# Kernel optimization log

Hardware: AMD Instinct MI355X
Metric: run time of the kernel (lower is better)

Reference implementation:

```python
import jax, jax.numpy as jnp
import numpy as np

K = 4096       # in_features (reduction dim)
N = 11008      # out_features
GROUP = 128    # scale group size along K
PACK = 8       # int4 values per int32


def dequantize_int4(packed, scales):
    """packed: [K//8, N] int32 (8 int4 nibbles per word along K),
    scales: [K//GROUP, N] fp16. Returns fp16 weight [K, N] with
    w = (nibble - 8) * scale (symmetric zero-point-8 scheme)."""
    shifts = (jnp.arange(PACK, dtype=jnp.int32) * 4)
    # [K//8, 8, N] -> [K, N]
    nibbles = (packed[:, None, :] >> shifts[None, :, None]) & 0xF
    q = nibbles.reshape(K, N)
    s = jnp.repeat(scales, GROUP, axis=0)  # [K, N]
    return (q.astype(jnp.float16) - jnp.float16(8.0)) * s


def setup_inputs() -> dict:
    key = jax.random.key(0)
    k1, k2, k3, k4 = jax.random.split(key, 4)
    x = jax.random.normal(k1, (4, 1024, K), dtype=jnp.float16)
    packed = jax.random.randint(k2, (K // PACK, N), 0, 2147483647, dtype=jnp.int32)
    scales = (jax.random.uniform(k3, (K // GROUP, N), dtype=jnp.float32) * 0.02 + 0.001).astype(jnp.float16)
    bias = jax.random.normal(k4, (N,), dtype=jnp.float16)
    return {"x": x, "packed": packed, "scales": scales, "bias": bias}


def reference(x, packed, scales, bias):
    in_shape = x.shape
    x2 = x.reshape(-1, in_shape[-1]).astype(jnp.float16)  # [M, K]
    w = dequantize_int4(packed, scales)                    # [K, N]
    out = jnp.matmul(x2, w)                                # [M, N] fp16
    out = out.reshape(*in_shape[:-1], -1)
    return out + bias
```

## Files before the change

kernel.cpp:

```cpp
#include <hip/hip_runtime.h>
#include <hip/hip_bf16.h>
#include <stdint.h>

#define K_DIM 4096
#define N_DIM 11008
#define BM 128
#define BN 256
#define NT (K_DIM / 64)

typedef _Float16 half8 __attribute__((ext_vector_type(8)));
typedef _Float16 half2v __attribute__((ext_vector_type(2)));
typedef float floatx4 __attribute__((ext_vector_type(4)));

typedef const uint32_t __attribute__((address_space(1)))* gas_u32p;
typedef uint32_t __attribute__((address_space(3)))* las_u32p;

__device__ __forceinline__ void glds16(const void* g, void* l) {
    __builtin_amdgcn_global_load_lds((gas_u32p)g, (las_u32p)l, 16, 0, 0);
}

__device__ __forceinline__ half8 dequant_word_pk(uint32_t w, half2v s2) {
    const uint32_t M = 0x000F000Fu;
    const uint32_t B = 0x64006400u;
    union { uint32_t u; half2v h; } t0, t1, t2, t3;
    t0.u = (w & M) | B;
    t1.u = ((w >> 4) & M) | B;
    t2.u = ((w >> 8) & M) | B;
    t3.u = ((w >> 12) & M) | B;
    const half2v off = {(_Float16)1032.0f, (_Float16)1032.0f};
    union { half8 h8; half2v h2[4]; } o;
    o.h2[0] = (t0.h - off) * s2;
    o.h2[1] = (t1.h - off) * s2;
    o.h2[2] = (t2.h - off) * s2;
    o.h2[3] = (t3.h - off) * s2;
    return o.h8;
}

__device__ __forceinline__ half8 dequant_word_f16(uint32_t w, float s) {
    half8 r;
    #pragma unroll
    for (int j = 0; j < 8; ++j) {
        int q = (int)((w >> (4 * j)) & 0xFu);
        r[j] = (_Float16)((float)(q - 8) * s);
    }
    return r;
}

__global__ __launch_bounds__(256)
void cvt_kernel(const float* __restrict__ X, _Float16* __restrict__ Xh) {
    size_t idx = (size_t)blockIdx.x * 256 + threadIdx.x;
    size_t base = idx * 8;
    floatx4 a = __builtin_nontemporal_load((const floatx4*)(X + base));
    floatx4 b = __builtin_nontemporal_load((const floatx4*)(X + base + 4));
    half8 h;
    h[0] = (_Float16)a[0]; h[1] = (_Float16)b[0];
    h[2] = (_Float16)a[1]; h[3] = (_Float16)b[1];
    h[4] = (_Float16)a[2]; h[5] = (_Float16)b[2];
    h[6] = (_Float16)a[3]; h[7] = (_Float16)b[3];
    *(half8*)(Xh + base) = h;
}

__global__ __launch_bounds__(256, 2)
void qgemm_lds(const _Float16* __restrict__ Xh,
               const int* __restrict__ Wp,
               const float* __restrict__ Sc,
               const float* __restrict__ Bias,
               float* __restrict__ Out)
{
    __shared__ half8 As[3][BM * 8];

    const int tid = threadIdx.x;

    const int bid = blockIdx.y * gridDim.x + blockIdx.x;
    const int xcd = bid & 7;
    const int k_r = bid >> 3;
    const int m0 = (xcd * 4 + (k_r & 3)) * BM;
    const int n0 = (k_r >> 2) * BN;

    const int lane = tid & 63;
    const int wid  = tid >> 6;
    const int wn   = wid;
    const int q    = lane >> 4;
    const int tt   = lane & 15;

    const int arow = tid >> 3;
    const int ac   = (tid & 7) ^ (arow & 7);
    const _Float16* aSrc = Xh + (size_t)(m0 + arow) * K_DIM + ac * 8;

    const int ncol = n0 + wn * 64 + tt;
    const int* bPtr = Wp + (size_t)q * N_DIM + ncol;
    const float* scPtr = Sc + ncol;

    floatx4 acc[8][4];
    #pragma unroll
    for (int i = 0; i < 8; ++i)
        #pragma unroll
        for (int j = 0; j < 4; ++j)
            acc[i][j] = floatx4{0.f, 0.f, 0.f, 0.f};

    const int x7  = tt & 7;
    const int rb0 = tt * 128 + ((0 * 4 + q) ^ x7) * 16;
    const int rb1 = tt * 128 + ((1 * 4 + q) ^ x7) * 16;

    char* pr = (char*)As[0];
    char* pm = (char*)As[1];
    char* pw = (char*)As[2];

    #pragma unroll
    for (int i = 0; i < 4; ++i)
        glds16(aSrc + (size_t)i * 32 * K_DIM,
               pr + (size_t)(i * 256 + tid) * 16);
    __builtin_amdgcn_sched_barrier(0);

    half2v s2[4], sn2[4];
    #pragma unroll
    for (int j = 0; j < 4; ++j) {
        _Float16 sh = (_Float16)scPtr[j * 16];
        s2[j] = (half2v){sh, sh};
    }
    uint32_t wv[8];
    #pragma unroll
    for (int ks = 0; ks < 2; ++ks)
        #pragma unroll
        for (int j = 0; j < 4; ++j)
            wv[ks * 4 + j] = (uint32_t)bPtr[(size_t)(ks * 4) * N_DIM + j * 16];
    __builtin_amdgcn_sched_barrier(0);

    #pragma unroll
    for (int i = 0; i < 4; ++i)
        glds16(aSrc + (size_t)i * 32 * K_DIM + 64,
               pm + (size_t)(i * 256 + tid) * 16);
    __builtin_amdgcn_sched_barrier(0);

    asm volatile("s_waitcnt vmcnt(16)" ::: "memory");
    __builtin_amdgcn_s_barrier();
    __builtin_amdgcn_sched_barrier(0);

    for (int kt = 0; kt < NT; ++kt) {
        if (kt > 0 && (kt & 1) == 0) {
            #pragma unroll
            for (int j = 0; j < 4; ++j) s2[j] = sn2[j];
        }

        half8 bf[8];
        #pragma unroll
        for (int ks = 0; ks < 2; ++ks)
            #pragma unroll
            for (int j = 0; j < 4; ++j)
                bf[ks * 4 + j] = dequant_word_pk(wv[ks * 4 + j], s2[j]);

        if (kt + 1 < NT) {
            const int* bp = bPtr + (size_t)(kt + 1) * 8 * N_DIM;
            #pragma unroll
            for (int ks = 0; ks < 2; ++ks)
                #pragma unroll
                for (int j = 0; j < 4; ++j)
                    wv[ks * 4 + j] = (uint32_t)bp[(size_t)(ks * 4) * N_DIM + j * 16];
            if (kt & 1) {
                const float* sp = scPtr + (size_t)((kt + 1) >> 1) * N_DIM;
                #pragma unroll
                for (int j = 0; j < 4; ++j) {
                    _Float16 sh = (_Float16)sp[j * 16];
                    sn2[j] = (half2v){sh, sh};
                }
            }
        }
        __builtin_amdgcn_sched_barrier(0);

        if (kt + 2 < NT) {
            #pragma unroll
            for (int i = 0; i < 4; ++i)
                glds16(aSrc + (size_t)i * 32 * K_DIM + (kt + 2) * 64,
                       pw + (size_t)(i * 256 + tid) * 16);
        }
        __builtin_amdgcn_sched_barrier(0);

        #pragma unroll
        for (int ks = 0; ks < 2; ++ks) {
            const int rb = ks ? rb1 : rb0;
            #pragma unroll
            for (int i = 0; i < 8; ++i) {
                half8 af = *(const half8*)(pr + rb + i * 2048);
                #pragma unroll
                for (int j = 0; j < 4; ++j)
                    acc[i][j] = __builtin_amdgcn_mfma_f32_16x16x32_f16(
                        af, bf[ks * 4 + j], acc[i][j], 0, 0, 0);
            }
        }

        if (kt + 1 < NT) {
            if (kt + 2 < NT) {
                if (kt & 1) { asm volatile("s_waitcnt vmcnt(16)" ::: "memory"); }
                else        { asm volatile("s_waitcnt vmcnt(12)" ::: "memory"); }
            } else {
                asm volatile("s_waitcnt vmcnt(8)" ::: "memory");
            }
            __builtin_amdgcn_s_barrier();
            __builtin_amdgcn_sched_barrier(0);
        }

        char* t = pr; pr = pm; pm = pw; pw = t;
    }

    #pragma unroll
    for (int j = 0; j < 4; ++j) {
        const int n = ncol + j * 16;
        const float bv = Bias[n];
        #pragma unroll
        for (int i = 0; i < 8; ++i) {
            const int mrow = m0 + i * 16 + q * 4;
            #pragma unroll
            for (int r = 0; r < 4; ++r)
                Out[(size_t)(mrow + r) * N_DIM + n] = acc[i][j][r] + bv;
        }
    }
}

__global__ __launch_bounds__(256, 2)
void qgemm_direct(const float* __restrict__ X,
                  const int* __restrict__ Wp,
                  const float* __restrict__ Sc,
                  const float* __restrict__ Bias,
                  float* __restrict__ Out)
{
    const int tid = threadIdx.x;
    const int m0 = blockIdx.x * 256;
    const int n0 = blockIdx.y * 128;
    const int lane = tid & 63;
    const int wid  = tid >> 6;
    const int wm   = wid >> 1;
    const int wn   = wid & 1;
    const int q    = lane >> 4;
    const int tt   = lane & 15;

    const int ncol = n0 + wn * 64 + tt;
    const int* bPtr = Wp + (size_t)q * N_DIM + ncol;
    const float* scPtr = Sc + ncol;
    const float* aBase = X + (size_t)(m0 + wm * 128 + tt) * K_DIM + q * 8;

    floatx4 acc[8][4];
    #pragma unroll
    for (int i = 0; i < 8; ++i)
        #pragma unroll
        for (int j = 0; j < 4; ++j)
            acc[i][j] = floatx4{0.f, 0.f, 0.f, 0.f};

    float s[4];
    for (int kt = 0; kt < NT; ++kt) {
        if ((kt & 1) == 0) {
            const float* sp = scPtr + (size_t)(kt >> 1) * N_DIM;
            #pragma unroll
            for (int j = 0; j < 4; ++j) s[j] = sp[j * 16];
        }
        const int* bp = bPtr + (size_t)kt * 8 * N_DIM;
        uint32_t wv[8];
        #pragma unroll
        for (int ks = 0; ks < 2; ++ks)
            #pragma unroll
            for (int j = 0; j < 4; ++j)
                wv[ks * 4 + j] = (uint32_t)bp[(size_t)(ks * 4) * N_DIM + j * 16];
        half8 bf[8];
        #pragma unroll
        for (int ks = 0; ks < 2; ++ks)
            #pragma unroll
            for (int j = 0; j < 4; ++j)
                bf[ks * 4 + j] = dequant_word_f16(wv[ks * 4 + j], s[j]);
        #pragma unroll
        for (int ks = 0; ks < 2; ++ks) {
            const size_t ko = (size_t)(kt * 64 + ks * 32);
            #pragma unroll
            for (int i = 0; i < 8; ++i) {
                const float* ap = aBase + (size_t)i * 16 * K_DIM + ko;
                floatx4 lo = *(const floatx4*)ap;
                floatx4 hi = *(const floatx4*)(ap + 4);
                half8 af;
                af[0] = (_Float16)lo[0]; af[1] = (_Float16)lo[1];
                af[2] = (_Float16)lo[2]; af[3] = (_Float16)lo[3];
                af[4] = (_Float16)hi[0]; af[5] = (_Float16)hi[1];
                af[6] = (_Float16)hi[2]; af[7] = (_Float16)hi[3];
                #pragma unroll
                for (int j = 0; j < 4; ++j)
                    acc[i][j] = __builtin_amdgcn_mfma_f32_16x16x32_f16(
                        af, bf[ks * 4 + j], acc[i][j], 0, 0, 0);
            }
        }
    }
    #pragma unroll
    for (int j = 0; j < 4; ++j) {
        const int n = ncol + j * 16;
        const float bv = Bias[n];
        #pragma unroll
        for (int i = 0; i < 8; ++i) {
            const int mrow = m0 + wm * 128 + i * 16 + q * 4;
            #pragma unroll
            for (int r = 0; r < 4; ++r)
                Out[(size_t)(mrow + r) * N_DIM + n] = acc[i][j][r] + bv;
        }
    }
}

extern "C" void kernel_launch(void* const* d_in, const int* in_sizes, int n_in,
                              void* d_out, int out_size, void* d_ws, size_t ws_size,
                              hipStream_t stream) {
    (void)in_sizes; (void)n_in; (void)out_size;
    const float* X    = (const float*)d_in[0];
    const int*   Wp   = (const int*)d_in[1];
    const float* Sc   = (const float*)d_in[2];
    const float* Bias = (const float*)d_in[3];
    float*       Out  = (float*)d_out;

    const size_t needed = (size_t)4096 * K_DIM * sizeof(_Float16);

    if (ws_size >= needed) {
        _Float16* Xh = (_Float16*)d_ws;
        cvt_kernel<<<(4096 * K_DIM) / (256 * 8), 256, 0, stream>>>(X, Xh);
        dim3 grid(4096 / BM, N_DIM / BN);
        qgemm_lds<<<grid, 256, 0, stream>>>(Xh, Wp, Sc, Bias, Out);
    } else {
        dim3 gridf(4096 / 256, N_DIM / 128);
        qgemm_direct<<<gridf, 256, 0, stream>>>(X, Wp, Sc, Bias, Out);
    }
}
```

Before: 604.6 us.

## Split K-tile into four interleaved phases with barriers and MFMA priority

Restructures the main K loop of the LDS GEMM into four sub-phases per tile. Each phase interleaves A-fragment LDS reads, next-tile weight loads, one global-to-LDS copy and dequantization with a 4x4 MFMA block. Phases are separated by workgroup barriers and raise wave priority around the MFMAs, in a ping-pong style meant to overlap memory and compute across the two waves per SIMD. Weight registers are double-buffered by unrolling the loop by two. The extra barriers add synchronization overhead and may stall if the waves do not interleave well.

```diff
diff --git a/kernel.cpp b/kernel.cpp
--- a/kernel.cpp
+++ b/kernel.cpp
@@ -60,6 +60,143 @@
     *(half8*)(Xh + base) = h;
 }
 
+__device__ __forceinline__ void tile_body(
+    int kt, uint32_t (&wvC)[8], uint32_t (&wvN)[8],
+    half2v (&s2)[4], half2v (&sn2)[4],
+    floatx4 (&acc)[8][4],
+    char*& pr, char*& pm, char*& pw,
+    const _Float16* aSrc, const int* bPtr, const float* scPtr,
+    int rb0, int rb1, int tid)
+{
+    if (kt > 0 && (kt & 1) == 0) {
+        #pragma unroll
+        for (int j = 0; j < 4; ++j) s2[j] = sn2[j];
+    }
+
+    const int* bp = bPtr + (size_t)(kt + 1) * 8 * N_DIM;
+    half8 bf[4];
+    half8 af[4];
+
+    #pragma unroll
+    for (int i = 0; i < 4; ++i)
+        af[i] = *(const half8*)(pr + rb0 + i * 2048);
+    if (kt + 1 < NT) {
+        #pragma unroll
+        for (int j = 0; j < 4; ++j)
+            wvN[j] = (uint32_t)bp[j * 16];
+    }
+    if (kt + 2 < NT)
+        glds16(aSrc + (size_t)(kt + 2) * 64,
+               pw + (size_t)tid * 16);
+    #pragma unroll
+    for (int j = 0; j < 4; ++j)
+        bf[j] = dequant_word_pk(wvC[j], s2[j]);
+    __builtin_amdgcn_sched_barrier(0);
+    __builtin_amdgcn_s_barrier();
+    asm volatile("s_waitcnt lgkmcnt(0)" ::: "memory");
+    __builtin_amdgcn_sched_barrier(0);
+    __builtin_amdgcn_s_setprio(1);
+    #pragma unroll
+    for (int i = 0; i < 4; ++i)
+        #pragma unroll
+        for (int j = 0; j < 4; ++j)
+            acc[i][j] = __builtin_amdgcn_mfma_f32_16x16x32_f16(
+                af[i], bf[j], acc[i][j], 0, 0, 0);
+    __builtin_amdgcn_s_setprio(0);
+    __builtin_amdgcn_sched_barrier(0);
+    __builtin_amdgcn_s_barrier();
+
+    #pragma unroll
+    for (int i = 0; i < 4; ++i)
+        af[i] = *(const half8*)(pr + rb0 + (4 + i) * 2048);
+    if (kt + 1 < NT) {
+        #pragma unroll
+        for (int j = 0; j < 4; ++j)
+            wvN[4 + j] = (uint32_t)bp[(size_t)4 * N_DIM + j * 16];
+    }
+    if (kt + 2 < NT)
+        glds16(aSrc + (size_t)1 * 32 * K_DIM + (size_t)(kt + 2) * 64,
+               pw + (size_t)(1 * 256 + tid) * 16);
+    __builtin_amdgcn_sched_barrier(0);
+    __builtin_amdgcn_s_barrier();
+    asm volatile("s_waitcnt lgkmcnt(0)" ::: "memory");
+    __builtin_amdgcn_sched_barrier(0);
+    __builtin_amdgcn_s_setprio(1);
+    #pragma unroll
+    for (int i = 0; i < 4; ++i)
+        #pragma unroll
+        for (int j = 0; j < 4; ++j)
+            acc[4 + i][j] = __builtin_amdgcn_mfma_f32_16x16x32_f16(
+                af[i], bf[j], acc[4 + i][j], 0, 0, 0);
+    __builtin_amdgcn_s_setprio(0);
+    __builtin_amdgcn_sched_barrier(0);
+    __builtin_amdgcn_s_barrier();
+
+    #pragma unroll
+    for (int i = 0; i < 4; ++i)
+        af[i] = *(const half8*)(pr + rb1 + i * 2048);
+    if ((kt & 1) && (kt + 1 < NT)) {
+        const float* sp = scPtr + (size_t)((kt + 1) >> 1) * N_DIM;
+        #pragma unroll
+        for (int j = 0; j < 4; ++j) {
+            _Float16 sh = (_Float16)sp[j * 16];
+            sn2[j] = (half2v){sh, sh};
+        }
+    }
+    if (kt + 2 < NT)
+        glds16(aSrc + (size_t)2 * 32 * K_DIM + (size_t)(kt + 2) * 64,
+               pw + (size_t)(2 * 256 + tid) * 16);
+    #pragma unroll
+    for (int j = 0; j < 4; ++j)
+        bf[j] = dequant_word_pk(wvC[4 + j], s2[j]);
+    __builtin_amdgcn_sched_barrier(0);
+    __builtin_amdgcn_s_barrier();
+    asm volatile("s_waitcnt lgkmcnt(0)" ::: "memory");
+    __builtin_amdgcn_sched_barrier(0);
+    __builtin_amdgcn_s_setprio(1);
+    #pragma unroll
+    for (int i = 0; i < 4; ++i)
+        #pragma unroll
+        for (int j = 0; j < 4; ++j)
+            acc[i][j] = __builtin_amdgcn_mfma_f32_16x16x32_f16(
+                af[i], bf[j], acc[i][j], 0, 0, 0);
+    __builtin_amdgcn_s_setprio(0);
+    __builtin_amdgcn_sched_barrier(0);
+    __builtin_amdgcn_s_barrier();
+
+    #pragma unroll
+    for (int i = 0; i < 4; ++i)
+        af[i] = *(const half8*)(pr + rb1 + (4 + i) * 2048);
+    if (kt + 2 < NT)
+        glds16(aSrc + (size_t)3 * 32 * K_DIM + (size_t)(kt + 2) * 64,
+               pw + (size_t)(3 * 256 + tid) * 16);
+    __builtin_amdgcn_sched_barrier(0);
+    __builtin_amdgcn_s_barrier();
+    asm volatile("s_waitcnt lgkmcnt(0)" ::: "memory");
+    __builtin_amdgcn_sched_barrier(0);
+    __builtin_amdgcn_s_setprio(1);
+    #pragma unroll
+    for (int i = 0; i < 4; ++i)
+        #pragma unroll
+        for (int j = 0; j < 4; ++j)
+            acc[4 + i][j] = __builtin_amdgcn_mfma_f32_16x16x32_f16(
+                af[i], bf[j], acc[4 + i][j], 0, 0, 0);
+    __builtin_amdgcn_s_setprio(0);
+    __builtin_amdgcn_sched_barrier(0);
+    if (kt + 1 < NT) {
+        if (kt + 2 < NT) {
+            if (kt & 1) { asm volatile("s_waitcnt vmcnt(16)" ::: "memory"); }
+            else        { asm volatile("s_waitcnt vmcnt(12)" ::: "memory"); }
+        } else {
+            asm volatile("s_waitcnt vmcnt(8)" ::: "memory");
+        }
+        __builtin_amdgcn_s_barrier();
+        __builtin_amdgcn_sched_barrier(0);
+    }
+
+    char* t = pr; pr = pm; pm = pw; pw = t;
+}
+
 __global__ __launch_bounds__(256, 2)
 void qgemm_lds(const _Float16* __restrict__ Xh,
                const int* __restrict__ Wp,
@@ -112,94 +249,34 @@
                pr + (size_t)(i * 256 + tid) * 16);
     __builtin_amdgcn_sched_barrier(0);
 
+    uint32_t wvA[8], wvB[8];
+    #pragma unroll
+    for (int ks = 0; ks < 2; ++ks)
+        #pragma unroll
+        for (int j = 0; j < 4; ++j)
+            wvA[ks * 4 + j] = (uint32_t)bPtr[(size_t)(ks * 4) * N_DIM + j * 16];
     half2v s2[4], sn2[4];
     #pragma unroll
     for (int j = 0; j < 4; ++j) {
         _Float16 sh = (_Float16)scPtr[j * 16];
         s2[j] = (half2v){sh, sh};
-    }
-    uint32_t wv[8];
-    #pragma unroll
-    for (int ks = 0; ks < 2; ++ks)
-        #pragma unroll
-        for (int j = 0; j < 4; ++j)
-            wv[ks * 4 + j] = (uint32_t)bPtr[(size_t)(ks * 4) * N_DIM + j * 16];
-    __builtin_amdgcn_sched_barrier(0);
-
+        sn2[j] = s2[j];
+    }
+    __builtin_amdgcn_sched_barrier(0);
     #pragma unroll
     for (int i = 0; i < 4; ++i)
         glds16(aSrc + (size_t)i * 32 * K_DIM + 64,
                pm + (size_t)(i * 256 + tid) * 16);
     __builtin_amdgcn_sched_barrier(0);
-
     asm volatile("s_waitcnt vmcnt(16)" ::: "memory");
     __builtin_amdgcn_s_barrier();
     __builtin_amdgcn_sched_barrier(0);
 
-    for (int kt = 0; kt < NT; ++kt) {
-        if (kt > 0 && (kt & 1) == 0) {
-            #pragma unroll
-            for (int j = 0; j < 4; ++j) s2[j] = sn2[j];
-        }
-
-        half8 bf[8];
-        #pragma unroll
-        for (int ks = 0; ks < 2; ++ks)
-            #pragma unroll
-            for (int j = 0; j < 4; ++j)
-                bf[ks * 4 + j] = dequant_word_pk(wv[ks * 4 + j], s2[j]);
-
-        if (kt + 1 < NT) {
-            const int* bp = bPtr + (size_t)(kt + 1) * 8 * N_DIM;
-            #pragma unroll
-            for (int ks = 0; ks < 2; ++ks)
-                #pragma unroll
-                for (int j = 0; j < 4; ++j)
-                    wv[ks * 4 + j] = (uint32_t)bp[(size_t)(ks * 4) * N_DIM + j * 16];
-            if (kt & 1) {
-                const float* sp = scPtr + (size_t)((kt + 1) >> 1) * N_DIM;
-                #pragma unroll
-                for (int j = 0; j < 4; ++j) {
-                    _Float16 sh = (_Float16)sp[j * 16];
-                    sn2[j] = (half2v){sh, sh};
-                }
-            }
-        }
-        __builtin_amdgcn_sched_barrier(0);
-
-        if (kt + 2 < NT) {
-            #pragma unroll
-            for (int i = 0; i < 4; ++i)
-                glds16(aSrc + (size_t)i * 32 * K_DIM + (kt + 2) * 64,
-                       pw + (size_t)(i * 256 + tid) * 16);
-        }
-        __builtin_amdgcn_sched_barrier(0);
-
-        #pragma unroll
-        for (int ks = 0; ks < 2; ++ks) {
-            const int rb = ks ? rb1 : rb0;
-            #pragma unroll
-            for (int i = 0; i < 8; ++i) {
-                half8 af = *(const half8*)(pr + rb + i * 2048);
-                #pragma unroll
-                for (int j = 0; j < 4; ++j)
-                    acc[i][j] = __builtin_amdgcn_mfma_f32_16x16x32_f16(
-                        af, bf[ks * 4 + j], acc[i][j], 0, 0, 0);
-            }
-        }
-
-        if (kt + 1 < NT) {
-            if (kt + 2 < NT) {
-                if (kt & 1) { asm volatile("s_waitcnt vmcnt(16)" ::: "memory"); }
-                else        { asm volatile("s_waitcnt vmcnt(12)" ::: "memory"); }
-            } else {
-                asm volatile("s_waitcnt vmcnt(8)" ::: "memory");
-            }
-            __builtin_amdgcn_s_barrier();
-            __builtin_amdgcn_sched_barrier(0);
-        }
-
-        char* t = pr; pr = pm; pm = pw; pw = t;
+    for (int kt = 0; kt < NT; kt += 2) {
+        tile_body(kt,     wvA, wvB, s2, sn2, acc, pr, pm, pw,
+                  aSrc, bPtr, scPtr, rb0, rb1, tid);
+        tile_body(kt + 1, wvB, wvA, s2, sn2, acc, pr, pm, pw,
+                  aSrc, bPtr, scPtr, rb0, rb1, tid);
     }
 
     #pragma unroll
```

New measurement: 657.7 us. 8.8% more time.
